# Kernel optimization log

Measured on AMD Instinct MI355X. Metric: run time of the kernel, lower is better.

## Reference

```python
import jax, jax.numpy as jnp
import numpy as np

B, S, D, H = 2, 2048, 1024, 16
DK = D // H


def setup_inputs() -> dict:
    key = jax.random.key(0)
    ks = jax.random.split(key, 9)
    def xavier(k, shape):
        fan_in, fan_out = shape[1], shape[0]
        lim = jnp.sqrt(6.0 / (fan_in + fan_out))
        return jax.random.uniform(k, shape, jnp.float32, -lim, lim)
    x = jax.random.normal(ks[0], (B, S, D), jnp.float32)
    mask = jnp.ones((B, 1, S), jnp.int32)
    Wq = xavier(ks[1], (D, D)); bq = jnp.zeros((D,), jnp.float32)
    Wk = xavier(ks[2], (D, D)); bk = jnp.zeros((D,), jnp.float32)
    Wv = xavier(ks[3], (D, D)); bv = jnp.zeros((D,), jnp.float32)
    Wo = xavier(ks[4], (D, D)); bo = jnp.zeros((D,), jnp.float32)
    return {"x": x, "mask": mask, "Wq": Wq, "bq": bq, "Wk": Wk, "bk": bk,
            "Wv": Wv, "bv": bv, "Wo": Wo, "bo": bo}


def reference(x, mask, Wq, bq, Wk, bk, Wv, bv, Wo, bo):
    # Linear layers use torch convention y = x @ W.T + b
    q = (x @ Wq.T + bq).reshape(B, S, H, DK).transpose(0, 2, 1, 3)  # [B,H,S,DK]
    k = (x @ Wk.T + bk).reshape(B, S, H, DK).transpose(0, 2, 1, 3)
    v = (x @ Wv.T + bv).reshape(B, S, H, DK).transpose(0, 2, 1, 3)
    scores = jnp.einsum('bhqd,bhkd->bhqk', q, k) / jnp.sqrt(jnp.float32(DK))
    m = mask[:, None, :, :]  # unsqueeze(1): broadcast over heads -> [B,1,1,S]
    scores = jnp.where(m == 0, jnp.float32(-1e9), scores)
    p = jax.nn.softmax(scores, axis=-1)  # dropout p=0.0 -> identity
    ctx = jnp.einsum('bhqk,bhkd->bhqd', p, v)
    ctx = ctx.transpose(0, 2, 1, 3).reshape(B, S, D)
    return ctx @ Wo.T + bo
```

## Files before the change

kernel.cpp:

```cpp
#include <hip/hip_runtime.h>
#include <hip/hip_bf16.h>
#include <math.h>

#define Bn 2
#define Sn 2048
#define Dn 1024
#define Hn 16
#define DKn 64
#define BHS (Bn * Hn * Sn)

using fragb  = __attribute__((ext_vector_type(8))) short;
using frag16 = __attribute__((ext_vector_type(8))) _Float16;
using f4     = __attribute__((ext_vector_type(4))) float;

__device__ __forceinline__ short f2bf(float f) {
    union { float f; unsigned u; } v; v.f = f;
    unsigned r = v.u + 0x7FFF + ((v.u >> 16) & 1);
    return (short)(r >> 16);
}
__device__ __forceinline__ unsigned short f2h(float f) {
    _Float16 h = (_Float16)f;
    unsigned short s; __builtin_memcpy(&s, &h, 2); return s;
}

#define GLOAD(gptr, lptr)                                                     \
    __builtin_amdgcn_global_load_lds(                                         \
        (const __attribute__((address_space(1))) unsigned int*)(const void*)(gptr), \
        (__attribute__((address_space(3))) unsigned int*)(void*)(lptr), 16, 0, 0)

#define NX (Bn * Sn * Dn)
#define NW (Dn * Dn)
#define NF4 ((NX + 4 * NW) / 4)

__global__ __launch_bounds__(256) void prep(
    const float* __restrict__ x,  const float* __restrict__ Wq,
    const float* __restrict__ Wk, const float* __restrict__ Wv,
    const float* __restrict__ Wo, const int* __restrict__ mask,
    short* __restrict__ xh,
    short* __restrict__ Wqh, short* __restrict__ Wkh,
    short* __restrict__ Wvh, short* __restrict__ Woh,
    short* __restrict__ mfb)
{
    int i = blockIdx.x * 256 + threadIdx.x;
    if (i < NF4) {
        int e = i << 2;
        const float* src; short* dst; int j;
        if (e < NX)               { src = x;  dst = xh;  j = e; }
        else if (e < NX + NW)     { src = Wq; dst = Wqh; j = e - NX; }
        else if (e < NX + 2 * NW) { src = Wk; dst = Wkh; j = e - NX - NW; }
        else if (e < NX + 3 * NW) { src = Wv; dst = Wvh; j = e - NX - 2 * NW; }
        else                      { src = Wo; dst = Woh; j = e - NX - 3 * NW; }
        float4 v = *(const float4*)(src + j);
        ushort4 o;
        o.x = f2h(v.x); o.y = f2h(v.y); o.z = f2h(v.z); o.w = f2h(v.w);
        *(ushort4*)(dst + j) = o;
    } else {
        int j = (i - NF4) << 2;
        if (j < Bn * Sn) {
            int4 m = *(const int4*)(mask + j);
            ushort4 o;
            o.x = m.x ? 0x3F80 : 0; o.y = m.y ? 0x3F80 : 0;
            o.z = m.z ? 0x3F80 : 0; o.w = m.w ? 0x3F80 : 0;
            *(ushort4*)(mfb + j) = o;
        }
    }
}


__global__ __launch_bounds__(256) void gemm_qkv(
    const short* __restrict__ A,
    const short* __restrict__ W0, const float* __restrict__ b0,
    const short* __restrict__ W1, const float* __restrict__ b1,
    const short* __restrict__ W2, const float* __restrict__ b2,
    const int* __restrict__ mask,
    short* __restrict__ Qb, short* __restrict__ Kb, short* __restrict__ Vtb)
{
    __shared__ __align__(16) short As0[128 * 32];
    __shared__ __align__(16) short Bs0[128 * 32];
    __shared__ __align__(16) short As1[128 * 32];
    __shared__ __align__(16) short Bs1[128 * 32];

    const int tid  = threadIdx.x;
    const int wave = tid >> 6;
    const int lane = tid & 63;
    const int quad = lane >> 4;
    const int l16  = lane & 15;
    const int wm   = wave >> 1;
    const int wn   = wave & 1;

    const int orig = blockIdx.y * 24 + blockIdx.x;
    const int swz  = (orig & 7) * 96 + (orig >> 3);
    const int by   = swz / 24;
    const int bx   = swz - by * 24;
    const int m0   = by * 128;
    const int n0   = bx * 128;
    const int widx = n0 >> 10;
    const int nl0  = n0 & 1023;

    const short* Wp   = widx == 0 ? W0 : (widx == 1 ? W1 : W2);
    const float* bias = widx == 0 ? b0 : (widx == 1 ? b1 : b2);

    f4 acc[4][4];
    #pragma unroll
    for (int i = 0; i < 4; i++)
        #pragma unroll
        for (int j = 0; j < 4; j++) {
            acc[i][j][0] = 0.f; acc[i][j][1] = 0.f;
            acc[i][j][2] = 0.f; acc[i][j][3] = 0.f;
        }

    const int K  = Dn;
    const int r0 = tid >> 2;
    const int sc = ((tid & 3) ^ ((tid >> 3) & 3)) * 8;
    const short* Ar0 = A  + (size_t)(m0  + r0)      * K + sc;
    const short* Ar1 = A  + (size_t)(m0  + r0 + 64) * K + sc;
    const short* Br0 = Wp + (size_t)(nl0 + r0)      * K + sc;
    const short* Br1 = Wp + (size_t)(nl0 + r0 + 64) * K + sc;

    const int cA = (quad ^ ((l16 >> 1) & 3)) * 8;

#define STAGEQ(AS, BS, kk) do {                                               \
    GLOAD(Ar0 + (kk), &AS[wave * 512]);                                       \
    GLOAD(Ar1 + (kk), &AS[2048 + wave * 512]);                                \
    GLOAD(Br0 + (kk), &BS[wave * 512]);                                       \
    GLOAD(Br1 + (kk), &BS[2048 + wave * 512]);                                \
} while (0)

#define COMPUTEQ(AS, BS) do {                                                 \
    frag16 a_[4], b_[4];                                                      \
    _Pragma("unroll")                                                         \
    for (int mi = 0; mi < 4; mi++)                                            \
        a_[mi] = *(const frag16*)&AS[(wm * 64 + mi * 16 + l16) * 32 + cA];    \
    _Pragma("unroll")                                                         \
    for (int ni = 0; ni < 4; ni++)                                            \
        b_[ni] = *(const frag16*)&BS[(wn * 64 + ni * 16 + l16) * 32 + cA];    \
    _Pragma("unroll")                                                         \
    for (int mi = 0; mi < 4; mi++)                                            \
        _Pragma("unroll")                                                     \
        for (int ni = 0; ni < 4; ni++)                                        \
            acc[mi][ni] = __builtin_amdgcn_mfma_f32_16x16x32_f16(             \
                a_[mi], b_[ni], acc[mi][ni], 0, 0, 0);                        \
} while (0)

    STAGEQ(As0, Bs0, 0);
    __syncthreads();
    for (int k0 = 0; k0 < K - 64; k0 += 64) {
        STAGEQ(As1, Bs1, k0 + 32);
        COMPUTEQ(As0, Bs0);
        __syncthreads();
        STAGEQ(As0, Bs0, k0 + 64);
        COMPUTEQ(As1, Bs1);
        __syncthreads();
    }
    STAGEQ(As1, Bs1, K - 32);
    COMPUTEQ(As0, Bs0);
    __syncthreads();
    COMPUTEQ(As1, Bs1);

    const float QSCALE = 0.125f * 1.44269504088896340736f;

    #pragma unroll
    for (int mi = 0; mi < 4; mi++) {
        #pragma unroll
        for (int ni = 0; ni < 4; ni++) {
            int nl = nl0 + wn * 64 + ni * 16 + l16;
            float bv = bias[nl];
            #pragma unroll
            for (int r = 0; r < 4; r++) {
                int m = m0 + wm * 64 + mi * 16 + quad * 4 + r;
                float v = acc[mi][ni][r] + bv;
                int b  = m >> 11, s = m & (Sn - 1);
                int h  = nl >> 6, dk = nl & 63;
                if (widx == 0)
                    Qb[((size_t)(b * Hn + h) * Sn + s) * DKn + dk] = f2bf(v * QSCALE);
                else if (widx == 1)
                    Kb[((size_t)(b * Hn + h) * Sn + s) * DKn + dk] = f2bf(v);
                else {
                    float mv = (float)mask[b * Sn + s];
                    Vtb[((size_t)(b * Hn + h) * DKn + dk) * Sn + s] = f2bf(v * mv);
                }
            }
        }
    }
}

__global__ __launch_bounds__(256) void gemm_out(
    const short* __restrict__ A, const short* __restrict__ Wp,
    const float* __restrict__ bias, float* __restrict__ outf)
{
    __shared__ __align__(16) short As0[64 * 32];
    __shared__ __align__(16) short Bs0[128 * 32];
    __shared__ __align__(16) short As1[64 * 32];
    __shared__ __align__(16) short Bs1[128 * 32];

    const int tid  = threadIdx.x;
    const int wave = tid >> 6;
    const int lane = tid & 63;
    const int quad = lane >> 4;
    const int l16  = lane & 15;
    const int wm   = wave >> 1;
    const int wn   = wave & 1;

    const int orig = blockIdx.y * 8 + blockIdx.x;
    const int swz  = (orig & 7) * 64 + (orig >> 3);
    const int m0   = (swz >> 3) * 64;
    const int n0   = (swz & 7) * 128;

    f4 acc[2][4];
    #pragma unroll
    for (int i = 0; i < 2; i++)
        #pragma unroll
        for (int j = 0; j < 4; j++) {
            acc[i][j][0] = 0.f; acc[i][j][1] = 0.f;
            acc[i][j][2] = 0.f; acc[i][j][3] = 0.f;
        }

    const int K  = Dn;
    const int r0 = tid >> 2;
    const int sc = ((tid & 3) ^ ((tid >> 3) & 3)) * 8;
    const short* Ao0 = A  + (size_t)(m0 + r0)      * K + sc;
    const short* Bo0 = Wp + (size_t)(n0 + r0)      * K + sc;
    const short* Bo1 = Wp + (size_t)(n0 + r0 + 64) * K + sc;

    const int cA = (quad ^ ((l16 >> 1) & 3)) * 8;

#define STAGEO(AS, BS, kk) do {                                               \
    GLOAD(Ao0 + (kk), &AS[wave * 512]);                                       \
    GLOAD(Bo0 + (kk), &BS[wave * 512]);                                       \
    GLOAD(Bo1 + (kk), &BS[2048 + wave * 512]);                                \
} while (0)

#define COMPUTEO(AS, BS) do {                                                 \
    frag16 a_[2], b_[4];                                                      \
    _Pragma("unroll")                                                         \
    for (int mi = 0; mi < 2; mi++)                                            \
        a_[mi] = *(const frag16*)&AS[(wm * 32 + mi * 16 + l16) * 32 + cA];    \
    _Pragma("unroll")                                                         \
    for (int ni = 0; ni < 4; ni++)                                            \
        b_[ni] = *(const frag16*)&BS[(wn * 64 + ni * 16 + l16) * 32 + cA];    \
    _Pragma("unroll")                                                         \
    for (int mi = 0; mi < 2; mi++)                                            \
        _Pragma("unroll")                                                     \
        for (int ni = 0; ni < 4; ni++)                                        \
            acc[mi][ni] = __builtin_amdgcn_mfma_f32_16x16x32_f16(             \
                a_[mi], b_[ni], acc[mi][ni], 0, 0, 0);                        \
} while (0)

    STAGEO(As0, Bs0, 0);
    __syncthreads();
    for (int k0 = 0; k0 < K - 64; k0 += 64) {
        STAGEO(As1, Bs1, k0 + 32);
        COMPUTEO(As0, Bs0);
        __syncthreads();
        STAGEO(As0, Bs0, k0 + 64);
        COMPUTEO(As1, Bs1);
        __syncthreads();
    }
    STAGEO(As1, Bs1, K - 32);
    COMPUTEO(As0, Bs0);
    __syncthreads();
    COMPUTEO(As1, Bs1);

    #pragma unroll
    for (int mi = 0; mi < 2; mi++) {
        #pragma unroll
        for (int ni = 0; ni < 4; ni++) {
            int nl = n0 + wn * 64 + ni * 16 + l16;
            float bv = bias[nl];
            #pragma unroll
            for (int r = 0; r < 4; r++) {
                int m = m0 + wm * 32 + mi * 16 + quad * 4 + r;
                outf[(size_t)m * Dn + nl] = acc[mi][ni][r] + bv;
            }
        }
    }
}

#define LP  72

__global__ __launch_bounds__(256) void attn_mfma(
    const short* __restrict__ Qb, const short* __restrict__ Kb,
    const short* __restrict__ Vtb, const short* __restrict__ mfb,
    float* __restrict__ ctxp0, float* __restrict__ ctxp1,
    float* __restrict__ lp)
{
    __shared__ __align__(16) short Ks[64 * 64];
    __shared__ __align__(16) short Vs[64 * 64];
    __shared__ short Ps[4][32 * LP];
    __shared__ __align__(16) short mfs[64];

    const int tid  = threadIdx.x;
    const int wave = tid >> 6;
    const int lane = tid & 63;
    const int quad = lane >> 4;
    const int l16  = lane & 15;

    const int split = blockIdx.x & 1;
    const int rest  = blockIdx.x >> 1;
    const int qt  = rest & 15;
    const int bhh = rest >> 4;
    const int b   = bhh >> 4;
    const int h   = bhh & 15;

    fragb qf[2][2];
    #pragma unroll
    for (int w = 0; w < 2; w++) {
        int qrow = qt * 128 + wave * 32 + w * 16 + l16;
        const short* qptr = Qb + ((size_t)bhh * Sn + qrow) * DKn + quad * 8;
        qf[w][0] = *(const fragb*)(qptr);
        qf[w][1] = *(const fragb*)(qptr + 32);
    }

    f4 ctx[2][4];
    #pragma unroll
    for (int w = 0; w < 2; w++)
        #pragma unroll
        for (int dt = 0; dt < 4; dt++) {
            ctx[w][dt][0] = 0.f; ctx[w][dt][1] = 0.f;
            ctx[w][dt][2] = 0.f; ctx[w][dt][3] = 0.f;
        }
    f4 lacc[2];
    lacc[0][0] = 0.f; lacc[0][1] = 0.f; lacc[0][2] = 0.f; lacc[0][3] = 0.f;
    lacc[1] = lacc[0];

    const int lr = lane >> 3;
    const int sc = ((lane & 7) ^ lr) * 8;
    const short* Kg = Kb  + (size_t)bhh * Sn * DKn;
    const short* Vg = Vtb + (size_t)bhh * DKn * Sn;
    const short* mg = mfb + (size_t)b * Sn;

    const short* Ksrc = Kg + (size_t)(wave * 16 + lr) * DKn + sc;
    const short* Vsrc = Vg + (size_t)(wave * 16 + lr) * Sn + sc;

    const int c0 = ((quad ^ (l16 & 7)) * 8);

    const int kt0 = split * 16;
    for (int kt = kt0; kt < kt0 + 16; kt++) {
        __syncthreads();
        GLOAD(Ksrc + (size_t)kt * 4096,             &Ks[(wave * 16) * 64]);
        GLOAD(Ksrc + (size_t)kt * 4096 + 8 * DKn,   &Ks[(wave * 16 + 8) * 64]);
        GLOAD(Vsrc + (size_t)kt * 64,               &Vs[(wave * 16) * 64]);
        GLOAD(Vsrc + (size_t)kt * 64 + 8 * Sn,      &Vs[(wave * 16 + 8) * 64]);
        if (tid < 8)
            *(uint4*)&mfs[tid * 8] = *(const uint4*)(mg + kt * 64 + tid * 8);
        __syncthreads();

        #pragma unroll
        for (int t = 0; t < 4; t++) {
            fragb k0 = *(const fragb*)&Ks[(t * 16 + l16) * 64 + c0];
            fragb k1 = *(const fragb*)&Ks[(t * 16 + l16) * 64 + (c0 ^ 32)];
            #pragma unroll
            for (int w = 0; w < 2; w++) {
                f4 a; a[0] = 0.f; a[1] = 0.f; a[2] = 0.f; a[3] = 0.f;
                a = __builtin_amdgcn_mfma_f32_16x16x32_bf16(k0, qf[w][0], a, 0, 0, 0);
                a = __builtin_amdgcn_mfma_f32_16x16x32_bf16(k1, qf[w][1], a, 0, 0, 0);
                unsigned u0 = __float_as_uint(__builtin_amdgcn_exp2f(a[0]));
                unsigned u1 = __float_as_uint(__builtin_amdgcn_exp2f(a[1]));
                unsigned u2 = __float_as_uint(__builtin_amdgcn_exp2f(a[2]));
                unsigned u3 = __float_as_uint(__builtin_amdgcn_exp2f(a[3]));
                uint2 pw;
                pw.x = __builtin_amdgcn_perm(u1, u0, 0x07060302u);
                pw.y = __builtin_amdgcn_perm(u3, u2, 0x07060302u);
                *(uint2*)&Ps[wave][(w * 16 + l16) * LP + 16 * t + quad * 4] = pw;
            }
        }

        fragb p[2][2];
        #pragma unroll
        for (int w = 0; w < 2; w++) {
            p[w][0] = *(const fragb*)&Ps[wave][(w * 16 + l16) * LP + quad * 8];
            p[w][1] = *(const fragb*)&Ps[wave][(w * 16 + l16) * LP + quad * 8 + 32];
        }
        fragb m0 = *(const fragb*)&mfs[quad * 8];
        fragb m1 = *(const fragb*)&mfs[quad * 8 + 32];
        #pragma unroll
        for (int w = 0; w < 2; w++) {
            lacc[w] = __builtin_amdgcn_mfma_f32_16x16x32_bf16(p[w][0], m0, lacc[w], 0, 0, 0);
            lacc[w] = __builtin_amdgcn_mfma_f32_16x16x32_bf16(p[w][1], m1, lacc[w], 0, 0, 0);
        }
        #pragma unroll
        for (int dt = 0; dt < 4; dt++) {
            fragb v0 = *(const fragb*)&Vs[(dt * 16 + l16) * 64 + c0];
            fragb v1 = *(const fragb*)&Vs[(dt * 16 + l16) * 64 + (c0 ^ 32)];
            #pragma unroll
            for (int w = 0; w < 2; w++) {
                ctx[w][dt] = __builtin_amdgcn_mfma_f32_16x16x32_bf16(p[w][0], v0, ctx[w][dt], 0, 0, 0);
                ctx[w][dt] = __builtin_amdgcn_mfma_f32_16x16x32_bf16(p[w][1], v1, ctx[w][dt], 0, 0, 0);
            }
        }
    }

    float* cp  = split ? ctxp1 : ctxp0;
    float* lpp = lp + (size_t)split * BHS;
    #pragma unroll
    for (int w = 0; w < 2; w++)
        #pragma unroll
        for (int r = 0; r < 4; r++) {
            int row = qt * 128 + wave * 32 + w * 16 + quad * 4 + r;
            if (l16 == 0) lpp[(size_t)bhh * Sn + row] = lacc[w][r];
            #pragma unroll
            for (int dt = 0; dt < 4; dt++)
                cp[((size_t)(b * Sn + row)) * Dn + h * DKn + dt * 16 + l16] =
                    ctx[w][dt][r];
        }
}

__global__ __launch_bounds__(256) void reduce_ctx(
    const float* __restrict__ c0, const float* __restrict__ c1,
    const float* __restrict__ lp, short* __restrict__ Ch)
{
    int i4 = blockIdx.x * 256 + threadIdx.x;
    int e    = i4 << 2;
    int brow = e >> 10;
    int d    = e & 1023;
    int b    = brow >> 11;
    int row  = brow & (Sn - 1);
    int h    = d >> 6;
    size_t li = (size_t)(b * Hn + h) * Sn + row;
    float l = lp[li] + lp[BHS + li];
    float inv = 1.f / l;
    float4 v0 = ((const float4*)c0)[i4];
    float4 v1 = ((const float4*)c1)[i4];
    ushort4 o;
    o.x = f2h((v0.x + v1.x) * inv);
    o.y = f2h((v0.y + v1.y) * inv);
    o.z = f2h((v0.z + v1.z) * inv);
    o.w = f2h((v0.w + v1.w) * inv);
    ((ushort4*)Ch)[i4] = o;
}

extern "C" void kernel_launch(void* const* d_in, const int* in_sizes, int n_in,
                              void* d_out, int out_size, void* d_ws, size_t ws_size,
                              hipStream_t stream) {
    const float* x    = (const float*)d_in[0];
    const int*   mask = (const int*)d_in[1];
    const float* Wq   = (const float*)d_in[2];
    const float* bq   = (const float*)d_in[3];
    const float* Wk   = (const float*)d_in[4];
    const float* bk   = (const float*)d_in[5];
    const float* Wv   = (const float*)d_in[6];
    const float* bv   = (const float*)d_in[7];
    const float* Wo   = (const float*)d_in[8];
    const float* bo   = (const float*)d_in[9];
    float* out = (float*)d_out;

    char* ws = (char*)d_ws;
    const size_t MB = 1024u * 1024u;
    short* xh    = (short*)(ws + 0 * MB);
    short* Wqh   = (short*)(ws + 8 * MB);
    short* Wkh   = (short*)(ws + 10 * MB);
    short* Wvh   = (short*)(ws + 12 * MB);
    short* Qb    = (short*)(ws + 16 * MB);
    short* Kb    = (short*)(ws + 24 * MB);
    short* Vtb   = (short*)(ws + 32 * MB);
    float* ctxp0 = (float*)(ws + 0 * MB);
    float* ctxp1 = (float*)(ws + 40 * MB);
    short* Woh   = (short*)(ws + 56 * MB);
    float* lp    = (float*)(ws + 58 * MB);
    short* mfb   = (short*)(ws + 59 * MB);
    short* Ch    = (short*)(ws + 60 * MB);

    const int PRE = NF4 + (Bn * Sn) / 4;
    prep<<<(PRE + 255) / 256, 256, 0, stream>>>(
        x, Wq, Wk, Wv, Wo, mask, xh, Wqh, Wkh, Wvh, Woh, mfb);

    gemm_qkv<<<dim3(24, 32), 256, 0, stream>>>(
        xh, Wqh, bq, Wkh, bk, Wvh, bv, mask, Qb, Kb, Vtb);

    attn_mfma<<<dim3(Bn * Hn * (Sn / 128) * 2), 256, 0, stream>>>(
        Qb, Kb, Vtb, mfb, ctxp0, ctxp1, lp);

    reduce_ctx<<<dim3(NX / 4 / 256), 256, 0, stream>>>(ctxp0, ctxp1, lp, Ch);

    gemm_out<<<dim3(8, 64), 256, 0, stream>>>(Ch, Woh, bo, out);
}
```

Baseline: 229.3 us.

## Warp-specialize QKV and output GEMMs with dedicated producer and consumer waves

Both GEMM kernels now launch 512 threads: four producer waves issue the global-to-LDS loads and four consumer waves run the MFMA compute, alternating across double buffers separated by block barriers. The output GEMM tile shrinks from 64x128 to 64x64, doubling its grid. The block-index swizzle used for cache locality is removed in both kernels. The aim is to overlap loads with compute, at the cost of extra idle waves and registers, smaller per-block compute for the output GEMM, and possibly worse L2 reuse without the swizzle.

```diff
diff --git a/kernel.cpp b/kernel.cpp
--- a/kernel.cpp
+++ b/kernel.cpp
@@ -67,7 +67,7 @@
 }
 
 
-__global__ __launch_bounds__(256) void gemm_qkv(
+__global__ __launch_bounds__(512) void gemm_qkv(
     const short* __restrict__ A,
     const short* __restrict__ W0, const float* __restrict__ b0,
     const short* __restrict__ W1, const float* __restrict__ b1,
@@ -85,15 +85,13 @@
     const int lane = tid & 63;
     const int quad = lane >> 4;
     const int l16  = lane & 15;
-    const int wm   = wave >> 1;
-    const int wn   = wave & 1;
-
-    const int orig = blockIdx.y * 24 + blockIdx.x;
-    const int swz  = (orig & 7) * 96 + (orig >> 3);
-    const int by   = swz / 24;
-    const int bx   = swz - by * 24;
-    const int m0   = by * 128;
-    const int n0   = bx * 128;
+    const bool pw  = wave >= 4;
+    const int  cw  = wave & 3;
+    const int  wm  = cw >> 1;
+    const int  wn  = cw & 1;
+
+    const int m0   = blockIdx.y * 128;
+    const int n0   = blockIdx.x * 128;
     const int widx = n0 >> 10;
     const int nl0  = n0 & 1023;
 
@@ -109,9 +107,10 @@
             acc[i][j][2] = 0.f; acc[i][j][3] = 0.f;
         }
 
-    const int K  = Dn;
-    const int r0 = tid >> 2;
-    const int sc = ((tid & 3) ^ ((tid >> 3) & 3)) * 8;
+    const int K    = Dn;
+    const int stid = tid & 255;
+    const int r0   = stid >> 2;
+    const int sc   = ((stid & 3) ^ ((stid >> 3) & 3)) * 8;
     const short* Ar0 = A  + (size_t)(m0  + r0)      * K + sc;
     const short* Ar1 = A  + (size_t)(m0  + r0 + 64) * K + sc;
     const short* Br0 = Wp + (size_t)(nl0 + r0)      * K + sc;
@@ -120,10 +119,10 @@
     const int cA = (quad ^ ((l16 >> 1) & 3)) * 8;
 
 #define STAGEQ(AS, BS, kk) do {                                               \
-    GLOAD(Ar0 + (kk), &AS[wave * 512]);                                       \
-    GLOAD(Ar1 + (kk), &AS[2048 + wave * 512]);                                \
-    GLOAD(Br0 + (kk), &BS[wave * 512]);                                       \
-    GLOAD(Br1 + (kk), &BS[2048 + wave * 512]);                                \
+    GLOAD(Ar0 + (kk), &AS[cw * 512]);                                         \
+    GLOAD(Ar1 + (kk), &AS[2048 + cw * 512]);                                  \
+    GLOAD(Br0 + (kk), &BS[cw * 512]);                                         \
+    GLOAD(Br1 + (kk), &BS[2048 + cw * 512]);                                  \
 } while (0)
 
 #define COMPUTEQ(AS, BS) do {                                                 \
@@ -142,19 +141,17 @@
                 a_[mi], b_[ni], acc[mi][ni], 0, 0, 0);                        \
 } while (0)
 
-    STAGEQ(As0, Bs0, 0);
+    if (pw) STAGEQ(As0, Bs0, 0);
     __syncthreads();
-    for (int k0 = 0; k0 < K - 64; k0 += 64) {
-        STAGEQ(As1, Bs1, k0 + 32);
-        COMPUTEQ(As0, Bs0);
-        __syncthreads();
-        STAGEQ(As0, Bs0, k0 + 64);
-        COMPUTEQ(As1, Bs1);
-        __syncthreads();
-    }
-    STAGEQ(As1, Bs1, K - 32);
-    COMPUTEQ(As0, Bs0);
+    for (int t = 0; t < 15; ++t) {
+        if (pw) STAGEQ(As1, Bs1, 64 * t + 32); else COMPUTEQ(As0, Bs0);
+        __syncthreads();
+        if (pw) STAGEQ(As0, Bs0, 64 * t + 64); else COMPUTEQ(As1, Bs1);
+        __syncthreads();
+    }
+    if (pw) STAGEQ(As1, Bs1, 992); else COMPUTEQ(As0, Bs0);
     __syncthreads();
+    if (pw) return;
     COMPUTEQ(As1, Bs1);
 
     const float QSCALE = 0.125f * 1.44269504088896340736f;
@@ -184,88 +181,85 @@
     }
 }
 
-__global__ __launch_bounds__(256) void gemm_out(
+__global__ __launch_bounds__(512) void gemm_out(
     const short* __restrict__ A, const short* __restrict__ Wp,
     const float* __restrict__ bias, float* __restrict__ outf)
 {
     __shared__ __align__(16) short As0[64 * 32];
-    __shared__ __align__(16) short Bs0[128 * 32];
+    __shared__ __align__(16) short Bs0[64 * 32];
     __shared__ __align__(16) short As1[64 * 32];
-    __shared__ __align__(16) short Bs1[128 * 32];
+    __shared__ __align__(16) short Bs1[64 * 32];
 
     const int tid  = threadIdx.x;
     const int wave = tid >> 6;
     const int lane = tid & 63;
     const int quad = lane >> 4;
     const int l16  = lane & 15;
-    const int wm   = wave >> 1;
-    const int wn   = wave & 1;
-
-    const int orig = blockIdx.y * 8 + blockIdx.x;
-    const int swz  = (orig & 7) * 64 + (orig >> 3);
-    const int m0   = (swz >> 3) * 64;
-    const int n0   = (swz & 7) * 128;
-
-    f4 acc[2][4];
+    const bool pw  = wave >= 4;
+    const int  cw  = wave & 3;
+    const int  wm  = cw >> 1;
+    const int  wn  = cw & 1;
+
+    const int m0 = blockIdx.y * 64;
+    const int n0 = blockIdx.x * 64;
+
+    f4 acc[2][2];
     #pragma unroll
     for (int i = 0; i < 2; i++)
         #pragma unroll
-        for (int j = 0; j < 4; j++) {
+        for (int j = 0; j < 2; j++) {
             acc[i][j][0] = 0.f; acc[i][j][1] = 0.f;
             acc[i][j][2] = 0.f; acc[i][j][3] = 0.f;
         }
 
-    const int K  = Dn;
-    const int r0 = tid >> 2;
-    const int sc = ((tid & 3) ^ ((tid >> 3) & 3)) * 8;
-    const short* Ao0 = A  + (size_t)(m0 + r0)      * K + sc;
-    const short* Bo0 = Wp + (size_t)(n0 + r0)      * K + sc;
-    const short* Bo1 = Wp + (size_t)(n0 + r0 + 64) * K + sc;
+    const int K    = Dn;
+    const int stid = tid & 255;
+    const int r0   = stid >> 2;
+    const int sc   = ((stid & 3) ^ ((stid >> 3) & 3)) * 8;
+    const short* Ao0 = A  + (size_t)(m0 + r0) * K + sc;
+    const short* Bo0 = Wp + (size_t)(n0 + r0) * K + sc;
 
     const int cA = (quad ^ ((l16 >> 1) & 3)) * 8;
 
 #define STAGEO(AS, BS, kk) do {                                               \
-    GLOAD(Ao0 + (kk), &AS[wave * 512]);                                       \
-    GLOAD(Bo0 + (kk), &BS[wave * 512]);                                       \
-    GLOAD(Bo1 + (kk), &BS[2048 + wave * 512]);                                \
+    GLOAD(Ao0 + (kk), &AS[cw * 512]);                                         \
+    GLOAD(Bo0 + (kk), &BS[cw * 512]);                                         \
 } while (0)
 
 #define COMPUTEO(AS, BS) do {                                                 \
-    frag16 a_[2], b_[4];                                                      \
+    frag16 a_[2], b_[2];                                                      \
     _Pragma("unroll")                                                         \
     for (int mi = 0; mi < 2; mi++)                                            \
         a_[mi] = *(const frag16*)&AS[(wm * 32 + mi * 16 + l16) * 32 + cA];    \
     _Pragma("unroll")                                                         \
-    for (int ni = 0; ni < 4; ni++)                                            \
-        b_[ni] = *(const frag16*)&BS[(wn * 64 + ni * 16 + l16) * 32 + cA];    \
+    for (int ni = 0; ni < 2; ni++)                                            \
+        b_[ni] = *(const frag16*)&BS[(wn * 32 + ni * 16 + l16) * 32 + cA];    \
     _Pragma("unroll")                                                         \
     for (int mi = 0; mi < 2; mi++)                                            \
         _Pragma("unroll")                                                     \
-        for (int ni = 0; ni < 4; ni++)                                        \
+        for (int ni = 0; ni < 2; ni++)                                        \
             acc[mi][ni] = __builtin_amdgcn_mfma_f32_16x16x32_f16(             \
                 a_[mi], b_[ni], acc[mi][ni], 0, 0, 0);                        \
 } while (0)
 
-    STAGEO(As0, Bs0, 0);
+    if (pw) STAGEO(As0, Bs0, 0);
     __syncthreads();
-    for (int k0 = 0; k0 < K - 64; k0 += 64) {
-        STAGEO(As1, Bs1, k0 + 32);
-        COMPUTEO(As0, Bs0);
-        __syncthreads();
-        STAGEO(As0, Bs0, k0 + 64);
-        COMPUTEO(As1, Bs1);
-        __syncthreads();
-    }
-    STAGEO(As1, Bs1, K - 32);
-    COMPUTEO(As0, Bs0);
+    for (int t = 0; t < 15; ++t) {
+        if (pw) STAGEO(As1, Bs1, 64 * t + 32); else COMPUTEO(As0, Bs0);
+        __syncthreads();
+        if (pw) STAGEO(As0, Bs0, 64 * t + 64); else COMPUTEO(As1, Bs1);
+        __syncthreads();
+    }
+    if (pw) STAGEO(As1, Bs1, 992); else COMPUTEO(As0, Bs0);
     __syncthreads();
+    if (pw) return;
     COMPUTEO(As1, Bs1);
 
     #pragma unroll
     for (int mi = 0; mi < 2; mi++) {
         #pragma unroll
-        for (int ni = 0; ni < 4; ni++) {
-            int nl = n0 + wn * 64 + ni * 16 + l16;
+        for (int ni = 0; ni < 2; ni++) {
+            int nl = n0 + wn * 32 + ni * 16 + l16;
             float bv = bias[nl];
             #pragma unroll
             for (int r = 0; r < 4; r++) {
@@ -464,7 +458,7 @@
     prep<<<(PRE + 255) / 256, 256, 0, stream>>>(
         x, Wq, Wk, Wv, Wo, mask, xh, Wqh, Wkh, Wvh, Woh, mfb);
 
-    gemm_qkv<<<dim3(24, 32), 256, 0, stream>>>(
+    gemm_qkv<<<dim3(24, 32), 512, 0, stream>>>(
         xh, Wqh, bq, Wkh, bk, Wvh, bv, mask, Qb, Kb, Vtb);
 
     attn_mfma<<<dim3(Bn * Hn * (Sn / 128) * 2), 256, 0, stream>>>(
@@ -472,5 +466,5 @@
 
     reduce_ctx<<<dim3(NX / 4 / 256), 256, 0, stream>>>(ctxp0, ctxp1, lp, Ch);
 
-    gemm_out<<<dim3(8, 64), 256, 0, stream>>>(Ch, Woh, bo, out);
-}
+    gemm_out<<<dim3(16, 64), 512, 0, stream>>>(Ch, Woh, bo, out);
+}
```

Result: slower. 234.7 us (+2.4%).
